# Optimization experiments

Measured on AMD Instinct MI355X. Metric: run time of the kernel, lower is better.

The kernel has to match this reference:

```python
import jax, jax.numpy as jnp
import numpy as np

GRID = (32, 32)       # SOM grid shape
INPUT_DIM = 512
BATCH = 16384
TAU = 0.5             # softmax temperature
EPS = 1e-8


def setup_inputs() -> dict:
    key = jax.random.key(0)
    k1, k2 = jax.random.split(key)
    x = jax.random.normal(k1, (BATCH, INPUT_DIM), dtype=jnp.float32)
    # glorot_uniform for shape (*GRID, INPUT_DIM): fan_in = 32*32, fan_out = 512
    fan_in, fan_out = GRID[0] * GRID[1], INPUT_DIM
    limit = float(np.sqrt(6.0 / (fan_in + fan_out)))
    weights_map = jax.random.uniform(
        k2, (*GRID, INPUT_DIM), dtype=jnp.float32, minval=-limit, maxval=limit
    )
    return {"x": x, "weights_map": weights_map}


def reference(x, weights_map):
    """SoftSOM forward: squared distances -> per-dimension softmax -> soft reconstruction."""
    B, D = x.shape
    gh, gw = GRID
    w_flat = weights_map.reshape(gh * gw, D)  # [N, D]
    d2 = (
        jnp.sum(x * x, axis=-1, keepdims=True)           # [B,1]
        + jnp.sum(w_flat * w_flat, axis=-1)[None, :]     # [1,N]
        - 2.0 * (x @ w_flat.T)                           # [B,N]
    )
    logits = (-d2 / TAU).reshape(B, gh, gw)
    # per-dimension softmax: softmax along each grid axis, combined multiplicatively
    s_rows = jax.nn.softmax(logits, axis=1)   # softmax over grid dim 0
    s_cols = jax.nn.softmax(logits, axis=2)   # softmax over grid dim 1
    a = s_rows * s_cols
    a = a / (jnp.sum(a, axis=(1, 2), keepdims=True) + EPS)  # renormalize over grid
    # soft reconstruction: weighted sum of prototypes
    y = jnp.einsum("bij,ijd->bd", a, weights_map)  # [B, D]
    return y
```

## Files before the change

### kernel.cpp

```cpp
#include <hip/hip_runtime.h>
#include <hip/hip_bf16.h>
#include <stdint.h>

#define B_SZ 16384
#define D_SZ 512
#define N_SZ 1024

using f16x8 = __attribute__((ext_vector_type(8))) _Float16;
using f16x4 = __attribute__((ext_vector_type(4))) _Float16;
using f32x4 = __attribute__((ext_vector_type(4))) float;

typedef unsigned int u32_as1 __attribute__((address_space(1)));
typedef unsigned int u32_as3 __attribute__((address_space(3)));

__device__ __forceinline__ void gload16(const void* g, void* lds_base) {
    __builtin_amdgcn_global_load_lds((const u32_as1*)g, (u32_as3*)lds_base, 16, 0, 0);
}

__global__ __launch_bounds__(256) void prep_w(
    const float* __restrict__ W, _Float16* __restrict__ wh,
    _Float16* __restrict__ wt, float* __restrict__ ww) {
    const int n = blockIdx.x;
    const int t = threadIdx.x;
    __shared__ float part[4];
    const float2 v = *reinterpret_cast<const float2*>(&W[(size_t)n * D_SZ + t * 2]);
    _Float16 h0 = (_Float16)v.x, h1 = (_Float16)v.y;
    wh[(size_t)n * D_SZ + t * 2] = h0;
    wh[(size_t)n * D_SZ + t * 2 + 1] = h1;
    wt[(size_t)(t * 2) * N_SZ + n] = h0;
    wt[(size_t)(t * 2 + 1) * N_SZ + n] = h1;
    float s = v.x * v.x + v.y * v.y;
    for (int o = 32; o; o >>= 1) s += __shfl_xor(s, o);
    if ((t & 63) == 0) part[t >> 6] = s;
    __syncthreads();
    if (t == 0) ww[n] = part[0] + part[1] + part[2] + part[3];
}

__global__ __launch_bounds__(256) void prep_x(
    const float* __restrict__ X, _Float16* __restrict__ xh) {
    const size_t idx = ((size_t)blockIdx.x * 256 + threadIdx.x) * 8;
    const float4 a = *reinterpret_cast<const float4*>(&X[idx]);
    const float4 b = *reinterpret_cast<const float4*>(&X[idx + 4]);
    f16x8 h = {(_Float16)a.x, (_Float16)a.y, (_Float16)a.z, (_Float16)a.w,
               (_Float16)b.x, (_Float16)b.y, (_Float16)b.z, (_Float16)b.w};
    *reinterpret_cast<f16x8*>(&xh[idx]) = h;
}

__global__ __launch_bounds__(256, 3) void gemm1(
    const _Float16* __restrict__ xh, const _Float16* __restrict__ wh,
    const float* __restrict__ ww, float* __restrict__ L) {
    __shared__ _Float16 As[2 * 128 * 32];
    __shared__ _Float16 Bs[2 * 128 * 32];
    const int tid = threadIdx.x;
    const int wid = tid >> 6, lane = tid & 63;
    const int raw = blockIdx.y * 8 + blockIdx.x;
    const int wsw = (raw & 7) * 128 + (raw >> 3);
    const int bn0 = (wsw & 7) * 128;
    const int bm0 = (wsw >> 3) * 128;
    const int m0 = (wid >> 1) * 64, n0 = (wid & 1) * 64;
    const int rA = lane & 15;
    const int cbr = (lane >> 4) * 16;
    const int rswz = ((rA >> 1) & 3) << 4;

    const int br0 = (wid * 2) * 16 + (lane >> 2);
    const int br1 = (wid * 2 + 1) * 16 + (lane >> 2);
    const int sg0 = ((lane & 3) ^ ((br0 >> 1) & 3)) * 8;
    const int sg1 = ((lane & 3) ^ ((br1 >> 1) & 3)) * 8;
    const int bdst0 = (wid * 2) * 1024;
    const int bdst1 = (wid * 2 + 1) * 1024;
    char* const As_b = (char*)As;
    char* const Bs_b = (char*)Bs;

    f32x4 acc[4][4];
    for (int mi = 0; mi < 4; ++mi)
        for (int ni = 0; ni < 4; ++ni) acc[mi][ni] = (f32x4){0.f, 0.f, 0.f, 0.f};

    gload16(&xh[(size_t)(bm0 + br0) * D_SZ + sg0], As_b + bdst0);
    gload16(&xh[(size_t)(bm0 + br1) * D_SZ + sg1], As_b + bdst1);
    gload16(&wh[(size_t)(bn0 + br0) * D_SZ + sg0], Bs_b + bdst0);
    gload16(&wh[(size_t)(bn0 + br1) * D_SZ + sg1], Bs_b + bdst1);
    __syncthreads();

    int cur = 0;
    for (int kt = 0; kt < 16; ++kt) {
        const int nxt = cur ^ 1;
        if (kt < 15) {
            const int gk = (kt + 1) * 32;
            gload16(&xh[(size_t)(bm0 + br0) * D_SZ + gk + sg0], As_b + nxt * 8192 + bdst0);
            gload16(&xh[(size_t)(bm0 + br1) * D_SZ + gk + sg1], As_b + nxt * 8192 + bdst1);
            gload16(&wh[(size_t)(bn0 + br0) * D_SZ + gk + sg0], Bs_b + nxt * 8192 + bdst0);
            gload16(&wh[(size_t)(bn0 + br1) * D_SZ + gk + sg1], Bs_b + nxt * 8192 + bdst1);
        }
        f16x8 af[4], bf[4];
        for (int mi = 0; mi < 4; ++mi)
            af[mi] = *reinterpret_cast<const f16x8*>(
                As_b + cur * 8192 + (m0 + mi * 16 + rA) * 64 + (cbr ^ rswz));
        for (int ni = 0; ni < 4; ++ni)
            bf[ni] = *reinterpret_cast<const f16x8*>(
                Bs_b + cur * 8192 + (n0 + ni * 16 + rA) * 64 + (cbr ^ rswz));
        for (int mi = 0; mi < 4; ++mi)
            for (int ni = 0; ni < 4; ++ni)
                acc[mi][ni] = __builtin_amdgcn_mfma_f32_16x16x32_f16(af[mi], bf[ni], acc[mi][ni], 0, 0, 0);
        __syncthreads();
        cur = nxt;
    }
    for (int mi = 0; mi < 4; ++mi)
        for (int ni = 0; ni < 4; ++ni) {
            const int nn = bn0 + n0 + ni * 16 + rA;
            const float wwn = ww[nn];
            const int bb = bm0 + m0 + mi * 16 + (lane >> 4) * 4;
            const f32x4 a = acc[mi][ni];
            for (int r = 0; r < 4; ++r)
                L[(size_t)(bb + r) * N_SZ + nn] = 4.f * a[r] - 2.f * wwn;
        }
}

__global__ __launch_bounds__(256) void softsm(float* __restrict__ L) {
    __shared__ float4 spart[4][8];
    __shared__ float mpart[4];
    __shared__ float Tp[4];
    const int t = threadIdx.x;
    const int w = t >> 6, lane = t & 63;
    const int g8 = t & 7;
    const int bid = blockIdx.x;
    const size_t row = (size_t)((bid & 7) * 2048 + (bid >> 3));
    const float4 v = *reinterpret_cast<const float4*>(&L[row * N_SZ + (size_t)t * 4]);

    float m = fmaxf(fmaxf(v.x, v.y), fmaxf(v.z, v.w));
    for (int o = 32; o; o >>= 1) m = fmaxf(m, __shfl_xor(m, o));
    if (lane == 0) mpart[w] = m;
    __syncthreads();
    m = fmaxf(fmaxf(mpart[0], mpart[1]), fmaxf(mpart[2], mpart[3]));

    const float u0 = __expf(v.x - m), u1 = __expf(v.y - m);
    const float u2 = __expf(v.z - m), u3 = __expf(v.w - m);
    float rs = (u0 + u1) + (u2 + u3);
    rs += __shfl_xor(rs, 1); rs += __shfl_xor(rs, 2); rs += __shfl_xor(rs, 4);
    float s0 = u0, s1 = u1, s2 = u2, s3 = u3;
    for (int o = 8; o <= 32; o <<= 1) {
        s0 += __shfl_xor(s0, o); s1 += __shfl_xor(s1, o);
        s2 += __shfl_xor(s2, o); s3 += __shfl_xor(s3, o);
    }
    if (lane < 8) spart[w][lane] = make_float4(s0, s1, s2, s3);
    __syncthreads();
    {
        const float4 q0 = spart[0][g8], q1 = spart[1][g8], q2 = spart[2][g8], q3 = spart[3][g8];
        s0 = (q0.x + q1.x) + (q2.x + q3.x);
        s1 = (q0.y + q1.y) + (q2.y + q3.y);
        s2 = (q0.z + q1.z) + (q2.z + q3.z);
        s3 = (q0.w + q1.w) + (q2.w + q3.w);
    }
    const float irs = __builtin_amdgcn_rcpf(rs);
    const float t0 = u0 * u0 * irs * __builtin_amdgcn_rcpf(s0);
    const float t1 = u1 * u1 * irs * __builtin_amdgcn_rcpf(s1);
    const float t2 = u2 * u2 * irs * __builtin_amdgcn_rcpf(s2);
    const float t3 = u3 * u3 * irs * __builtin_amdgcn_rcpf(s3);
    float sT = (t0 + t1) + (t2 + t3);
    for (int o = 1; o <= 32; o <<= 1) sT += __shfl_xor(sT, o);
    if (lane == 0) Tp[w] = sT;
    __syncthreads();
    const float T = (Tp[0] + Tp[1]) + (Tp[2] + Tp[3]);
    const float inv = __builtin_amdgcn_rcpf(T + 1e-8f);
    f16x4 o16 = {(_Float16)(t0 * inv), (_Float16)(t1 * inv),
                 (_Float16)(t2 * inv), (_Float16)(t3 * inv)};
    char* out = (char*)L + (row >> 1) * 8192 + 4096 + (row & 1) * 2048 + (size_t)t * 8;
    *reinterpret_cast<f16x4*>(out) = o16;
}

__global__ __launch_bounds__(256, 3) void gemm2(
    const char* __restrict__ aBytes, const _Float16* __restrict__ wt,
    float* __restrict__ Y) {
    __shared__ _Float16 As[2 * 128 * 32];
    __shared__ _Float16 Bs[2 * 128 * 32];
    const int tid = threadIdx.x;
    const int wid = tid >> 6, lane = tid & 63;
    const int raw = blockIdx.y * 4 + blockIdx.x;
    const int wsw = (raw & 7) * 64 + (raw >> 3);
    const int bn0 = (wsw & 3) * 128;
    const int bm0 = (wsw >> 2) * 128;
    const int m0 = (wid >> 1) * 64, n0 = (wid & 1) * 64;
    const int rA = lane & 15;
    const int cbr = (lane >> 4) * 16;
    const int rswz = ((rA >> 1) & 3) << 4;

    const int br0 = (wid * 2) * 16 + (lane >> 2);
    const int br1 = (wid * 2 + 1) * 16 + (lane >> 2);
    const int sg0 = ((lane & 3) ^ ((br0 >> 1) & 3)) * 8;
    const int sg1 = ((lane & 3) ^ ((br1 >> 1) & 3)) * 8;
    const int bdst0 = (wid * 2) * 1024;
    const int bdst1 = (wid * 2 + 1) * 1024;
    char* const As_b = (char*)As;
    char* const Bs_b = (char*)Bs;
    const int ab0 = bm0 + br0, ab1 = bm0 + br1;
    const size_t abase0 = (size_t)(ab0 >> 1) * 8192 + 4096 + (size_t)(ab0 & 1) * 2048;
    const size_t abase1 = (size_t)(ab1 >> 1) * 8192 + 4096 + (size_t)(ab1 & 1) * 2048;

    f32x4 acc[4][4];
    for (int mi = 0; mi < 4; ++mi)
        for (int ni = 0; ni < 4; ++ni) acc[mi][ni] = (f32x4){0.f, 0.f, 0.f, 0.f};

    gload16(aBytes + abase0 + (size_t)sg0 * 2, As_b + bdst0);
    gload16(aBytes + abase1 + (size_t)sg1 * 2, As_b + bdst1);
    gload16(&wt[(size_t)(bn0 + br0) * N_SZ + sg0], Bs_b + bdst0);
    gload16(&wt[(size_t)(bn0 + br1) * N_SZ + sg1], Bs_b + bdst1);
    __syncthreads();

    int cur = 0;
    for (int kt = 0; kt < 32; ++kt) {
        const int nxt = cur ^ 1;
        if (kt < 31) {
            const int gk = (kt + 1) * 32;
            gload16(aBytes + abase0 + (size_t)(gk + sg0) * 2, As_b + nxt * 8192 + bdst0);
            gload16(aBytes + abase1 + (size_t)(gk + sg1) * 2, As_b + nxt * 8192 + bdst1);
            gload16(&wt[(size_t)(bn0 + br0) * N_SZ + gk + sg0], Bs_b + nxt * 8192 + bdst0);
            gload16(&wt[(size_t)(bn0 + br1) * N_SZ + gk + sg1], Bs_b + nxt * 8192 + bdst1);
        }
        f16x8 af[4], bf[4];
        for (int mi = 0; mi < 4; ++mi)
            af[mi] = *reinterpret_cast<const f16x8*>(
                As_b + cur * 8192 + (m0 + mi * 16 + rA) * 64 + (cbr ^ rswz));
        for (int ni = 0; ni < 4; ++ni)
            bf[ni] = *reinterpret_cast<const f16x8*>(
                Bs_b + cur * 8192 + (n0 + ni * 16 + rA) * 64 + (cbr ^ rswz));
        for (int mi = 0; mi < 4; ++mi)
            for (int ni = 0; ni < 4; ++ni)
                acc[mi][ni] = __builtin_amdgcn_mfma_f32_16x16x32_f16(af[mi], bf[ni], acc[mi][ni], 0, 0, 0);
        __syncthreads();
        cur = nxt;
    }
    for (int mi = 0; mi < 4; ++mi)
        for (int ni = 0; ni < 4; ++ni) {
            const int dd = bn0 + n0 + ni * 16 + rA;
            const int bb = bm0 + m0 + mi * 16 + (lane >> 4) * 4;
            const f32x4 a = acc[mi][ni];
            for (int r = 0; r < 4; ++r)
                Y[(size_t)(bb + r) * D_SZ + dd] = a[r];
        }
}

extern "C" void kernel_launch(void* const* d_in, const int* in_sizes, int n_in,
                              void* d_out, int out_size, void* d_ws, size_t ws_size,
                              hipStream_t stream) {
    (void)in_sizes; (void)n_in; (void)out_size; (void)ws_size;
    const float* X = (const float*)d_in[0];
    const float* W = (const float*)d_in[1];
    float* Y = (float*)d_out;
    char* ws = (char*)d_ws;

    float* L = (float*)ws;
    _Float16* wh = (_Float16*)(ws + (size_t)64 * 1024 * 1024);
    _Float16* wt = wh + (size_t)N_SZ * D_SZ;
    float* ww = (float*)(wt + (size_t)N_SZ * D_SZ);
    _Float16* xh = (_Float16*)((char*)ww + 4096);

    prep_w<<<N_SZ, 256, 0, stream>>>(W, wh, wt, ww);
    prep_x<<<(B_SZ * D_SZ) / (256 * 8), 256, 0, stream>>>(X, xh);
    gemm1<<<dim3(N_SZ / 128, B_SZ / 128), 256, 0, stream>>>(xh, wh, ww, L);
    softsm<<<B_SZ, 256, 0, stream>>>(L);
    gemm2<<<dim3(D_SZ / 128, B_SZ / 128), 256, 0, stream>>>((const char*)L, wt, Y);
}
```

Baseline: 105.5 us.

## Store logits in fp16 via LDS-staged coalesced writes and merge prep kernels

```diff
diff --git a/kernel.cpp b/kernel.cpp
--- a/kernel.cpp
+++ b/kernel.cpp
@@ -17,40 +17,42 @@
     __builtin_amdgcn_global_load_lds((const u32_as1*)g, (u32_as3*)lds_base, 16, 0, 0);
 }
 
-__global__ __launch_bounds__(256) void prep_w(
-    const float* __restrict__ W, _Float16* __restrict__ wh,
-    _Float16* __restrict__ wt, float* __restrict__ ww) {
-    const int n = blockIdx.x;
+__global__ __launch_bounds__(256) void prep(
+    const float* __restrict__ W, const float* __restrict__ X,
+    _Float16* __restrict__ wh, _Float16* __restrict__ wt,
+    float* __restrict__ ww, _Float16* __restrict__ xh) {
+    __shared__ float part[4];
+    const int bid = blockIdx.x;
     const int t = threadIdx.x;
-    __shared__ float part[4];
-    const float2 v = *reinterpret_cast<const float2*>(&W[(size_t)n * D_SZ + t * 2]);
-    _Float16 h0 = (_Float16)v.x, h1 = (_Float16)v.y;
-    wh[(size_t)n * D_SZ + t * 2] = h0;
-    wh[(size_t)n * D_SZ + t * 2 + 1] = h1;
-    wt[(size_t)(t * 2) * N_SZ + n] = h0;
-    wt[(size_t)(t * 2 + 1) * N_SZ + n] = h1;
-    float s = v.x * v.x + v.y * v.y;
-    for (int o = 32; o; o >>= 1) s += __shfl_xor(s, o);
-    if ((t & 63) == 0) part[t >> 6] = s;
-    __syncthreads();
-    if (t == 0) ww[n] = part[0] + part[1] + part[2] + part[3];
-}
-
-__global__ __launch_bounds__(256) void prep_x(
-    const float* __restrict__ X, _Float16* __restrict__ xh) {
-    const size_t idx = ((size_t)blockIdx.x * 256 + threadIdx.x) * 8;
-    const float4 a = *reinterpret_cast<const float4*>(&X[idx]);
-    const float4 b = *reinterpret_cast<const float4*>(&X[idx + 4]);
-    f16x8 h = {(_Float16)a.x, (_Float16)a.y, (_Float16)a.z, (_Float16)a.w,
-               (_Float16)b.x, (_Float16)b.y, (_Float16)b.z, (_Float16)b.w};
-    *reinterpret_cast<f16x8*>(&xh[idx]) = h;
+    if (bid < N_SZ) {
+        const int n = bid;
+        const float2 v = *reinterpret_cast<const float2*>(&W[(size_t)n * D_SZ + t * 2]);
+        _Float16 h0 = (_Float16)v.x, h1 = (_Float16)v.y;
+        wh[(size_t)n * D_SZ + t * 2] = h0;
+        wh[(size_t)n * D_SZ + t * 2 + 1] = h1;
+        wt[(size_t)(t * 2) * N_SZ + n] = h0;
+        wt[(size_t)(t * 2 + 1) * N_SZ + n] = h1;
+        float s = v.x * v.x + v.y * v.y;
+        for (int o = 32; o; o >>= 1) s += __shfl_xor(s, o);
+        if ((t & 63) == 0) part[t >> 6] = s;
+        __syncthreads();
+        if (t == 0) ww[n] = part[0] + part[1] + part[2] + part[3];
+    } else {
+        const int b2 = bid - N_SZ;
+        const int chunk = (b2 & 7) * 512 + (b2 >> 3);
+        const size_t idx = ((size_t)chunk * 256 + t) * 8;
+        const float4 a = *reinterpret_cast<const float4*>(&X[idx]);
+        const float4 b = *reinterpret_cast<const float4*>(&X[idx + 4]);
+        f16x8 h = {(_Float16)a.x, (_Float16)a.y, (_Float16)a.z, (_Float16)a.w,
+                   (_Float16)b.x, (_Float16)b.y, (_Float16)b.z, (_Float16)b.w};
+        *reinterpret_cast<f16x8*>(&xh[idx]) = h;
+    }
 }
 
 __global__ __launch_bounds__(256, 3) void gemm1(
     const _Float16* __restrict__ xh, const _Float16* __restrict__ wh,
-    const float* __restrict__ ww, float* __restrict__ L) {
-    __shared__ _Float16 As[2 * 128 * 32];
-    __shared__ _Float16 Bs[2 * 128 * 32];
+    const float* __restrict__ ww, _Float16* __restrict__ L16) {
+    __shared__ _Float16 smem[16384];
     const int tid = threadIdx.x;
     const int wid = tid >> 6, lane = tid & 63;
     const int raw = blockIdx.y * 8 + blockIdx.x;
@@ -68,8 +70,8 @@
     const int sg1 = ((lane & 3) ^ ((br1 >> 1) & 3)) * 8;
     const int bdst0 = (wid * 2) * 1024;
     const int bdst1 = (wid * 2 + 1) * 1024;
-    char* const As_b = (char*)As;
-    char* const Bs_b = (char*)Bs;
+    char* const As_b = (char*)smem;
+    char* const Bs_b = (char*)smem + 16384;
 
     f32x4 acc[4][4];
     for (int mi = 0; mi < 4; ++mi)
@@ -104,18 +106,26 @@
         __syncthreads();
         cur = nxt;
     }
+
     for (int mi = 0; mi < 4; ++mi)
         for (int ni = 0; ni < 4; ++ni) {
-            const int nn = bn0 + n0 + ni * 16 + rA;
-            const float wwn = ww[nn];
-            const int bb = bm0 + m0 + mi * 16 + (lane >> 4) * 4;
+            const int ln = n0 + ni * 16 + rA;
+            const float wwn = ww[bn0 + ln];
+            const int lm = m0 + mi * 16 + (lane >> 4) * 4;
             const f32x4 a = acc[mi][ni];
             for (int r = 0; r < 4; ++r)
-                L[(size_t)(bb + r) * N_SZ + nn] = 4.f * a[r] - 2.f * wwn;
-        }
-}
-
-__global__ __launch_bounds__(256) void softsm(float* __restrict__ L) {
+                smem[(lm + r) * 128 + ln] = (_Float16)(4.f * a[r] - 2.f * wwn);
+        }
+    __syncthreads();
+    for (int c = 0; c < 8; ++c) {
+        const int idx = c * 2048 + tid * 8;
+        const int row = idx >> 7, col = idx & 127;
+        const f16x8 v = *reinterpret_cast<const f16x8*>(&smem[idx]);
+        *reinterpret_cast<f16x8*>(&L16[(size_t)(bm0 + row) * N_SZ + bn0 + col]) = v;
+    }
+}
+
+__global__ __launch_bounds__(256) void softsm(_Float16* __restrict__ L16) {
     __shared__ float4 spart[4][8];
     __shared__ float mpart[4];
     __shared__ float Tp[4];
@@ -124,16 +134,17 @@
     const int g8 = t & 7;
     const int bid = blockIdx.x;
     const size_t row = (size_t)((bid & 7) * 2048 + (bid >> 3));
-    const float4 v = *reinterpret_cast<const float4*>(&L[row * N_SZ + (size_t)t * 4]);
-
-    float m = fmaxf(fmaxf(v.x, v.y), fmaxf(v.z, v.w));
+    const f16x4 lv = *reinterpret_cast<const f16x4*>(&L16[row * N_SZ + (size_t)t * 4]);
+    const float v0 = (float)lv[0], v1 = (float)lv[1], v2 = (float)lv[2], v3 = (float)lv[3];
+
+    float m = fmaxf(fmaxf(v0, v1), fmaxf(v2, v3));
     for (int o = 32; o; o >>= 1) m = fmaxf(m, __shfl_xor(m, o));
     if (lane == 0) mpart[w] = m;
     __syncthreads();
     m = fmaxf(fmaxf(mpart[0], mpart[1]), fmaxf(mpart[2], mpart[3]));
 
-    const float u0 = __expf(v.x - m), u1 = __expf(v.y - m);
-    const float u2 = __expf(v.z - m), u3 = __expf(v.w - m);
+    const float u0 = __expf(v0 - m), u1 = __expf(v1 - m);
+    const float u2 = __expf(v2 - m), u3 = __expf(v3 - m);
     float rs = (u0 + u1) + (u2 + u3);
     rs += __shfl_xor(rs, 1); rs += __shfl_xor(rs, 2); rs += __shfl_xor(rs, 4);
     float s0 = u0, s1 = u1, s2 = u2, s3 = u3;
@@ -163,12 +174,11 @@
     const float inv = __builtin_amdgcn_rcpf(T + 1e-8f);
     f16x4 o16 = {(_Float16)(t0 * inv), (_Float16)(t1 * inv),
                  (_Float16)(t2 * inv), (_Float16)(t3 * inv)};
-    char* out = (char*)L + (row >> 1) * 8192 + 4096 + (row & 1) * 2048 + (size_t)t * 8;
-    *reinterpret_cast<f16x4*>(out) = o16;
+    *reinterpret_cast<f16x4*>(&L16[row * N_SZ + (size_t)t * 4]) = o16;
 }
 
 __global__ __launch_bounds__(256, 3) void gemm2(
-    const char* __restrict__ aBytes, const _Float16* __restrict__ wt,
+    const _Float16* __restrict__ a16, const _Float16* __restrict__ wt,
     float* __restrict__ Y) {
     __shared__ _Float16 As[2 * 128 * 32];
     __shared__ _Float16 Bs[2 * 128 * 32];
@@ -191,16 +201,13 @@
     const int bdst1 = (wid * 2 + 1) * 1024;
     char* const As_b = (char*)As;
     char* const Bs_b = (char*)Bs;
-    const int ab0 = bm0 + br0, ab1 = bm0 + br1;
-    const size_t abase0 = (size_t)(ab0 >> 1) * 8192 + 4096 + (size_t)(ab0 & 1) * 2048;
-    const size_t abase1 = (size_t)(ab1 >> 1) * 8192 + 4096 + (size_t)(ab1 & 1) * 2048;
 
     f32x4 acc[4][4];
     for (int mi = 0; mi < 4; ++mi)
         for (int ni = 0; ni < 4; ++ni) acc[mi][ni] = (f32x4){0.f, 0.f, 0.f, 0.f};
 
-    gload16(aBytes + abase0 + (size_t)sg0 * 2, As_b + bdst0);
-    gload16(aBytes + abase1 + (size_t)sg1 * 2, As_b + bdst1);
+    gload16(&a16[(size_t)(bm0 + br0) * N_SZ + sg0], As_b + bdst0);
+    gload16(&a16[(size_t)(bm0 + br1) * N_SZ + sg1], As_b + bdst1);
     gload16(&wt[(size_t)(bn0 + br0) * N_SZ + sg0], Bs_b + bdst0);
     gload16(&wt[(size_t)(bn0 + br1) * N_SZ + sg1], Bs_b + bdst1);
     __syncthreads();
@@ -210,8 +217,8 @@
         const int nxt = cur ^ 1;
         if (kt < 31) {
             const int gk = (kt + 1) * 32;
-            gload16(aBytes + abase0 + (size_t)(gk + sg0) * 2, As_b + nxt * 8192 + bdst0);
-            gload16(aBytes + abase1 + (size_t)(gk + sg1) * 2, As_b + nxt * 8192 + bdst1);
+            gload16(&a16[(size_t)(bm0 + br0) * N_SZ + gk + sg0], As_b + nxt * 8192 + bdst0);
+            gload16(&a16[(size_t)(bm0 + br1) * N_SZ + gk + sg1], As_b + nxt * 8192 + bdst1);
             gload16(&wt[(size_t)(bn0 + br0) * N_SZ + gk + sg0], Bs_b + nxt * 8192 + bdst0);
             gload16(&wt[(size_t)(bn0 + br1) * N_SZ + gk + sg1], Bs_b + nxt * 8192 + bdst1);
         }
@@ -247,15 +254,14 @@
     float* Y = (float*)d_out;
     char* ws = (char*)d_ws;
 
-    float* L = (float*)ws;
-    _Float16* wh = (_Float16*)(ws + (size_t)64 * 1024 * 1024);
-    _Float16* wt = wh + (size_t)N_SZ * D_SZ;
-    float* ww = (float*)(wt + (size_t)N_SZ * D_SZ);
-    _Float16* xh = (_Float16*)((char*)ww + 4096);
-
-    prep_w<<<N_SZ, 256, 0, stream>>>(W, wh, wt, ww);
-    prep_x<<<(B_SZ * D_SZ) / (256 * 8), 256, 0, stream>>>(X, xh);
-    gemm1<<<dim3(N_SZ / 128, B_SZ / 128), 256, 0, stream>>>(xh, wh, ww, L);
-    softsm<<<B_SZ, 256, 0, stream>>>(L);
-    gemm2<<<dim3(D_SZ / 128, B_SZ / 128), 256, 0, stream>>>((const char*)L, wt, Y);
-}
+    _Float16* L16 = (_Float16*)ws;
+    _Float16* wh  = (_Float16*)(ws + (size_t)32 * 1024 * 1024);
+    _Float16* wt  = (_Float16*)(ws + (size_t)33 * 1024 * 1024);
+    float*    ww  = (float*)   (ws + (size_t)34 * 1024 * 1024);
+    _Float16* xh  = (_Float16*)(ws + (size_t)34 * 1024 * 1024 + 4096);
+
+    prep<<<N_SZ + 4096, 256, 0, stream>>>(W, X, wh, wt, ww, xh);
+    gemm1<<<dim3(N_SZ / 128, B_SZ / 128), 256, 0, stream>>>(xh, wh, ww, L16);
+    softsm<<<B_SZ, 256, 0, stream>>>(L16);
+    gemm2<<<dim3(D_SZ / 128, B_SZ / 128), 256, 0, stream>>>(L16, wt, Y);
+}
```

New measurement: 99.54 us. -5.6%, faster.
